# Optimization experiments

Hardware: AMD Instinct MI355X
Metric: run time of the kernel (lower is better)

Reference implementation:

```python
import jax, jax.numpy as jnp
import numpy as np

B, D, T = 256, 128, 512
H = 512
E = 256
WSCALE = 0.05


def setup_inputs() -> dict:
    key = jax.random.key(0)
    ks = jax.random.split(key, 8)
    return {
        "z": jax.random.normal(ks[0], (B, D, T), dtype=jnp.float32),
        "e": jax.random.normal(ks[1], (B, E), dtype=jnp.float32),
        "W_ih": jax.random.normal(ks[2], (3 * H, D), dtype=jnp.float32) * WSCALE,
        "W_hh": jax.random.normal(ks[3], (3 * H, H), dtype=jnp.float32) * WSCALE,
        "b_ih": jax.random.normal(ks[4], (3 * H,), dtype=jnp.float32) * WSCALE,
        "b_hh": jax.random.normal(ks[5], (3 * H,), dtype=jnp.float32) * WSCALE,
        "fc_W": jax.random.normal(ks[6], (D, H), dtype=jnp.float32) * WSCALE,
        "fc_b": jax.random.normal(ks[7], (D,), dtype=jnp.float32) * WSCALE,
    }


def _gru_cell(x, h, W_ih, W_hh, b_ih, b_hh):
    # torch.nn.GRUCell math
    gi = x @ W_ih.T + b_ih  # [B, 3H]
    gh = h @ W_hh.T + b_hh  # [B, 3H]
    i_r, i_z, i_n = jnp.split(gi, 3, axis=-1)
    h_r, h_z, h_n = jnp.split(gh, 3, axis=-1)
    r = jax.nn.sigmoid(i_r + h_r)
    zg = jax.nn.sigmoid(i_z + h_z)
    n = jnp.tanh(i_n + r * h_n)
    return (1.0 - zg) * n + zg * h


def reference(z, e, W_ih, W_hh, b_ih, b_hh, fc_W, fc_b):
    Bd, Dd, Td = z.shape
    Hd = W_hh.shape[1]
    z0 = z[:, :, 0]  # [B, D]
    h0 = jnp.zeros((Bd, Hd), dtype=z.dtype)

    def step(carry, _):
        h_fast, z_prev = carry
        h_fast = _gru_cell(z_prev, h_fast, W_ih, W_hh, b_ih, b_hh)
        delta = h_fast @ fc_W.T + fc_b
        z_t = z_prev + delta
        return (h_fast, z_t), z_t

    _, zs = jax.lax.scan(step, (h0, z0), None, length=Td - 1)  # [T-1, B, D]
    z_hat = jnp.concatenate([z0[None], zs], axis=0)  # [T, B, D]
    return jnp.transpose(z_hat, (1, 2, 0))  # [B, D, T]
```

## Files before the change

### kernel.cpp

```cpp
#include <hip/hip_runtime.h>
#include <hip/hip_fp16.h>

typedef _Float16 f16x8 __attribute__((ext_vector_type(8)));
typedef float f32x4 __attribute__((ext_vector_type(4)));
typedef unsigned long long u64;

#define NT 512
#define B_ 256
#define D_ 128
#define T_ 512
#define H_ 512

#define NG 8
#define CB 32
#define BS 32
#define HS 16
#define DS 4
#define GHSZ (NG * BS * H_)

#define SC  2048.0f
#define S1  (1.0f/2048.0f)
#define S2  (1.0f/4194304.0f)

#define MFMA16(A,B,C) __builtin_amdgcn_mfma_f32_16x16x32_f16((A),(B),(C),0,0,0)
#define ALD(p)   __hip_atomic_load((p),  __ATOMIC_RELAXED, __HIP_MEMORY_SCOPE_AGENT)

__global__ __launch_bounds__(256)
void msd_setup_M(const float* __restrict__ W_ih, const float* __restrict__ fc_W,
                 _Float16* __restrict__ Mhi,
                 _Float16* __restrict__ Mlo)
{
    const int r0 = (blockIdx.x >> 1) * 4;
    const int k  = ((blockIdx.x & 1) << 8) + threadIdx.x;
    for (int rr = 0; rr < 4; ++rr) {
        const int R = r0 + rr;
        const float* wrow = W_ih + (size_t)R * D_;
        float s = 0.0f;
        for (int d = 0; d < D_; ++d) s = fmaf(wrow[d], fc_W[(size_t)d * H_ + k], s);
        _Float16 hi = (_Float16)s;
        _Float16 lo = (_Float16)((s - (float)hi) * SC);
        const int t = R >> 9, jj = R & 511;
        const int c = jj >> 4, l16 = jj & 15;
        const int kt = k >> 5, quad = (k >> 3) & 3, j = k & 7;
        const size_t off = ((size_t)(((c * 3 + t) * 16 + kt) * 16 + l16) * 4 + quad) * 8 + j;
        Mhi[off] = hi;
        Mlo[off] = lo;
    }
}

template<bool L> __device__ __forceinline__ u64 hld(const u64* p) {
    if constexpr (L) return *p;
    else return __hip_atomic_load(p, __ATOMIC_RELAXED, __HIP_MEMORY_SCOPE_AGENT);
}
template<bool L> __device__ __forceinline__ void hst(unsigned short* p, unsigned short v) {
    if constexpr (L) *p = v;
    else __hip_atomic_store(p, v, __ATOMIC_RELAXED, __HIP_MEMORY_SCOPE_AGENT);
}

template<bool L>
__device__ __forceinline__
void run_loop(float* __restrict__ out,
              unsigned short* __restrict__ h1_g, unsigned short* __restrict__ h2_g,
              const _Float16* __restrict__ Mhi_w, const _Float16* __restrict__ Mlo_w,
              unsigned* cg, const unsigned* flgW, volatile unsigned* flgPub,
              const _Float16* Whh_s, const _Float16* WhhL_s, const _Float16* fcW_s,
              float* scr0,
              const int g, const int B0, const int j0, const int d0,
              const int tid, const int lane, const int l16, const int quad,
              const int bh, const int kq, const int bm0,
              const int fcrow, const int* mtb,
              float zfrag, const float* gi0,
              const float* bhh_l, const float* c_l, const float fcb_l)
{
    float gi_st[3] = {gi0[0], gi0[1], gi0[2]};
    float h_own = 0.0f;
    const int ktb = kq * 4;
    const int r_own = bm0 + quad * 4 + kq;
    const size_t a64 = ((size_t)(bm0 + l16) * H_ + quad * 8) >> 2;

    f16x8 Mh[4][3], Ml[4][3];
    #pragma unroll
    for (int ktl = 0; ktl < 4; ++ktl)
        #pragma unroll
        for (int t = 0; t < 3; ++t) {
            Mh[ktl][t] = *(const f16x8*)(Mhi_w + mtb[t] + (ktb + ktl) * 512);
            Ml[ktl][t] = *(const f16x8*)(Mlo_w + mtb[t] + (ktb + ktl) * 512);
        }

    for (int i = 1; i <= T_; ++i) {
        const unsigned tgt = (unsigned)(i - 1);
        if constexpr (L) {
            const volatile unsigned* fp =
                (const volatile unsigned*)(flgW + (lane & 31));
            for (;;) {
                unsigned f = *fp;
                if (__ballot((int)(f >= tgt)) == ~0ull) break;
                asm volatile("buffer_inv" ::: "memory");
            }
            asm volatile("buffer_inv" ::: "memory");
        }

        const size_t rb = (size_t)((i - 1) & 1) * GHSZ + (size_t)g * (BS * H_);
        const size_t wb = (size_t)(i & 1) * GHSZ + (size_t)g * (BS * H_);
        const u64* rh1 = (const u64*)(h1_g + rb);
        const u64* rh2 = (const u64*)(h2_g + rb);

        u64 Ar[4][4];
        #pragma unroll
        for (int ktl = 0; ktl < 4; ++ktl) {
            const int ktg = ktb + ktl;
            Ar[ktl][0] = hld<L>(rh1 + a64 + ktg * 8);
            Ar[ktl][1] = hld<L>(rh1 + a64 + ktg * 8 + 1);
            Ar[ktl][2] = hld<L>(rh2 + a64 + ktg * 8);
            Ar[ktl][3] = hld<L>(rh2 + a64 + ktg * 8 + 1);
        }

        f32x4 acc_gh[3], acc2_gh[3], accM1[3], acc2_gi[3], acc_fc;
        {
            f32x4 z4 = {0.f, 0.f, 0.f, 0.f};
            #pragma unroll
            for (int t = 0; t < 3; ++t) { acc_gh[t] = z4; acc2_gh[t] = z4; accM1[t] = z4; acc2_gi[t] = z4; }
            acc_fc = z4;
        }

        #pragma unroll
        for (int ktl = 0; ktl < 4; ++ktl) {
            const int ktg = ktb + ktl;
            union { u64 q[2]; f16x8 v; } U1, U2;
            U1.q[0] = Ar[ktl][0]; U1.q[1] = Ar[ktl][1];
            U2.q[0] = Ar[ktl][2]; U2.q[1] = Ar[ktl][3];
            f16x8 Ah = U1.v;
            f16x8 Al = U2.v;
            const int chunk = ((ktg * 4 + quad) ^ (l16 & 7)) * 8;
            #pragma unroll
            for (int t = 0; t < 3; ++t) {
                const int row = (t * 16 + l16) * 512 + chunk;
                f16x8 Bwh = *(const f16x8*)(Whh_s + row);
                f16x8 Bwl = *(const f16x8*)(WhhL_s + row);
                acc_gh[t]  = MFMA16(Ah, Bwh, acc_gh[t]);
                acc2_gh[t] = MFMA16(Al, Bwh, acc2_gh[t]);
                acc2_gh[t] = MFMA16(Ah, Bwl, acc2_gh[t]);
                accM1[t]   = MFMA16(Ah, Mh[ktl][t], accM1[t]);
                acc2_gi[t] = MFMA16(Al, Mh[ktl][t], acc2_gi[t]);
                acc2_gi[t] = MFMA16(Ah, Ml[ktl][t], acc2_gi[t]);
            }
            f16x8 Bf = *(const f16x8*)(fcW_s + ((ktg * 4 + quad) ^ fcrow) * 8 + fcrow * 512);
            acc_fc = MFMA16(Ah, Bf, acc_fc);
        }

        float Pgh[3][4], Pgi[3][4], Pfc[4];
        #pragma unroll
        for (int t = 0; t < 3; ++t)
            #pragma unroll
            for (int e = 0; e < 4; ++e) {
                Pgh[t][e] = acc_gh[t][e] * S1 + acc2_gh[t][e] * S2;
                Pgi[t][e] = accM1[t][e] * S1 + acc2_gi[t][e] * S2;
            }
        #pragma unroll
        for (int e = 0; e < 4; ++e) Pfc[e] = acc_fc[e] * S1;

        #pragma unroll
        for (int e = 0; e < 4; ++e) {
            if (e == kq) continue;
            const int si = (kq < e) ? kq : kq - 1;
            float* sp = scr0 + ((((bh * 4 + e) * 3 + si) * 64 + lane) * 9);
            sp[0] = Pgh[0][e]; sp[1] = Pgh[1][e]; sp[2] = Pgh[2][e];
            sp[3] = Pgi[0][e]; sp[4] = Pgi[1][e]; sp[5] = Pgi[2][e];
            sp[6] = Pfc[e];
        }
        __syncthreads();
        float tgh0 = Pgh[0][kq], tgh1 = Pgh[1][kq], tgh2 = Pgh[2][kq];
        float tgi0 = Pgi[0][kq], tgi1 = Pgi[1][kq], tgi2 = Pgi[2][kq];
        float tfc  = Pfc[kq];
        #pragma unroll
        for (int s = 0; s < 3; ++s) {
            const float* sp = scr0 + ((((bh * 4 + kq) * 3 + s) * 64 + lane) * 9);
            tgh0 += sp[0]; tgh1 += sp[1]; tgh2 += sp[2];
            tgi0 += sp[3]; tgi1 += sp[4]; tgi2 += sp[5];
            tfc  += sp[6];
        }

        if (i >= 2) {
            gi_st[0] += tgi0 + c_l[0];
            gi_st[1] += tgi1 + c_l[1];
            gi_st[2] += tgi2 + c_l[2];
            if (l16 < DS) zfrag += tfc + fcb_l;
        }
        if (i <= T_ - 1) {
            float ghr = tgh0 + bhh_l[0];
            float ghz = tgh1 + bhh_l[1];
            float ghn = tgh2 + bhh_l[2];
            float r  = 1.0f / (1.0f + __expf(-(gi_st[0] + ghr)));
            float zg = 1.0f / (1.0f + __expf(-(gi_st[1] + ghz)));
            float xn = gi_st[2] + r * ghn;
            float hn = (1.0f - zg) * tanhf(xn) + zg * h_own;
            h_own = hn;
            const size_t o = (size_t)r_own * H_ + j0 + l16;
            float hs = hn * SC;
            _Float16 a1 = (_Float16)hs;
            _Float16 a2 = (_Float16)((hs - (float)a1) * SC);
            union { _Float16 f; unsigned short u; } c1, c2;
            c1.f = a1; c2.f = a2;
            hst<L>(h1_g + wb + o, c1.u);
            hst<L>(h2_g + wb + o, c2.u);
        }
        __syncthreads();
        if constexpr (L) {
            if (tid == 0) *flgPub = (unsigned)i;
        } else {
            if (tid == 0) {
                __hip_atomic_fetch_add(cg, 1u, __ATOMIC_RELAXED, __HIP_MEMORY_SCOPE_AGENT);
                const unsigned target = (unsigned)(CB * i);
                while (ALD(cg) < target) __builtin_amdgcn_s_sleep(1);
            }
            __syncthreads();
        }
        if (i >= 2 && l16 < DS)
            out[(size_t)(B0 + r_own) * (D_ * T_) + (size_t)(d0 + l16) * T_ + (i - 1)] = zfrag;
    }
}

__global__ __launch_bounds__(NT, 2)
void msd_gru_kernel(const float* __restrict__ zin,
                    const float* __restrict__ W_ih,
                    const float* __restrict__ W_hh,
                    const float* __restrict__ b_ih,
                    const float* __restrict__ b_hh,
                    const float* __restrict__ fc_W,
                    const float* __restrict__ fc_b,
                    float* __restrict__ out,
                    unsigned short* __restrict__ h1_g,
                    unsigned short* __restrict__ h2_g,
                    const _Float16* __restrict__ Mhi_w,
                    const _Float16* __restrict__ Mlo_w,
                    unsigned* __restrict__ cnt)
{
    const int g   = blockIdx.x & 7;
    const int c   = blockIdx.x >> 3;
    const int B0  = g * BS;
    const int j0  = c * HS;
    const int d0  = c * DS;

    const int tid  = threadIdx.x;
    const int wave = tid >> 6;
    const int lane = tid & 63;
    const int l16  = lane & 15;
    const int quad = lane >> 4;
    const int bh   = wave >> 2;
    const int kq   = wave & 3;
    const int bm0  = bh * 16;
    const int r_own = bm0 + quad * 4 + kq;

    __shared__ __attribute__((aligned(16))) _Float16 Whh_s [48 * 512];
    __shared__ __attribute__((aligned(16))) _Float16 WhhL_s[48 * 512];
    __shared__ __attribute__((aligned(16))) _Float16 fcW_s [4 * 512];
    __shared__ __attribute__((aligned(16))) float    scr   [2 * 4 * 3 * 64 * 9];
    __shared__ int mode_s;

    unsigned* xmask = cnt + 640;
    unsigned* ready = cnt + 768;
    if (tid == 0) {
        unsigned xcc;
        asm volatile("s_getreg_b32 %0, hwreg(HW_REG_XCC_ID)" : "=s"(xcc));
        __hip_atomic_fetch_or(xmask + g, 1u << (xcc & 31u), __ATOMIC_RELAXED, __HIP_MEMORY_SCOPE_AGENT);
        __hip_atomic_fetch_add(ready, 1u, __ATOMIC_RELAXED, __HIP_MEMORY_SCOPE_AGENT);
        while (ALD(ready) < (unsigned)(NG * CB)) __builtin_amdgcn_s_sleep(4);
        unsigned m = ALD(xmask + g);
        mode_s = (m & (m - 1u)) ? 1 : 0;
    }

    float* z0s = (float*)Whh_s;
    for (int idx = tid; idx < BS * D_; idx += NT) {
        int b = idx >> 7, d = idx & (D_ - 1);
        z0s[idx] = zin[(size_t)(B0 + b) * (D_ * T_) + (size_t)d * T_];
    }
    __syncthreads();

    float zfrag = (l16 < DS) ? z0s[r_own * D_ + d0 + l16] : 0.0f;
    if (l16 < DS)
        out[(size_t)(B0 + r_own) * (D_ * T_) + (size_t)(d0 + l16) * T_] = zfrag;
    float gi0[3], bhh_l[3], c_l[3];
    for (int t = 0; t < 3; ++t) {
        const int gr = t * H_ + j0 + l16;
        const float* wrow = W_ih + (size_t)gr * D_;
        bhh_l[t] = b_hh[gr];
        float s = b_ih[gr], cc = 0.0f;
        for (int d = 0; d < D_; ++d) {
            float wv = wrow[d];
            cc = fmaf(wv, fc_b[d], cc);
            s  = fmaf(wv, z0s[r_own * D_ + d], s);
        }
        c_l[t] = cc;
        gi0[t] = s;
    }
    const float fcb_l = (l16 < DS) ? fc_b[d0 + l16] : 0.0f;
    __syncthreads();

    for (int idx = tid; idx < 48 * H_; idx += NT) {
        int r = idx >> 9, k = idx & (H_ - 1);
        int gr = (r >> 4) * H_ + j0 + (r & 15);
        int pos = r * 512 + ((((k >> 3) ^ (r & 7)) << 3) | (k & 7));
        float w = W_hh[(size_t)gr * H_ + k];
        _Float16 hi = (_Float16)w;
        Whh_s [pos] = hi;
        WhhL_s[pos] = (_Float16)((w - (float)hi) * SC);
    }
    for (int idx = tid; idx < 4 * H_; idx += NT) {
        int r = idx >> 9, k = idx & (H_ - 1);
        int pos = r * 512 + ((((k >> 3) ^ r) << 3) | (k & 7));
        fcW_s[pos] = (_Float16)fc_W[(size_t)(d0 + r) * H_ + k];
    }
    __syncthreads();

    const int gmode = mode_s;
    const unsigned* flgW = cnt + g * 32;
    volatile unsigned* flgPub = (volatile unsigned*)(cnt + g * 32 + c);
    unsigned* cg = cnt + 256 + g * 32;
    const int fcrow = (l16 < DS) ? l16 : 0;
    int mtb[3];
    #pragma unroll
    for (int t = 0; t < 3; ++t) mtb[t] = ((c * 3 + t) * 16) * 512 + (l16 * 4 + quad) * 8;

    if (gmode == 0)
        run_loop<true >(out, h1_g, h2_g, Mhi_w, Mlo_w, cg, flgW, flgPub,
                        Whh_s, WhhL_s, fcW_s, scr,
                        g, B0, j0, d0, tid, lane, l16, quad, bh, kq, bm0,
                        fcrow, mtb, zfrag, gi0, bhh_l, c_l, fcb_l);
    else
        run_loop<false>(out, h1_g, h2_g, Mhi_w, Mlo_w, cg, flgW, flgPub,
                        Whh_s, WhhL_s, fcW_s, scr,
                        g, B0, j0, d0, tid, lane, l16, quad, bh, kq, bm0,
                        fcrow, mtb, zfrag, gi0, bhh_l, c_l, fcb_l);
}

extern "C" void kernel_launch(void* const* d_in, const int* in_sizes, int n_in,
                              void* d_out, int out_size, void* d_ws, size_t ws_size,
                              hipStream_t stream) {
    const float* z    = (const float*)d_in[0];
    const float* W_ih = (const float*)d_in[2];
    const float* W_hh = (const float*)d_in[3];
    const float* b_ih = (const float*)d_in[4];
    const float* b_hh = (const float*)d_in[5];
    const float* fc_W = (const float*)d_in[6];
    const float* fc_b = (const float*)d_in[7];
    float* out = (float*)d_out;

    char* w = (char*)d_ws;
    unsigned*       cnt = (unsigned*)w;
    unsigned short* h1  = (unsigned short*)(w + 4096);
    unsigned short* h2  = (unsigned short*)(w + 4096 + (size_t)4 * GHSZ);
    _Float16*       Mhi = (_Float16*)(w + 4096 + (size_t)8 * GHSZ);
    _Float16*       Mlo = (_Float16*)(w + 4096 + (size_t)8 * GHSZ + (size_t)3 * H_ * H_ * 2);

    hipMemsetAsync(d_ws, 0, 4096 + (size_t)8 * GHSZ, stream);

    hipLaunchKernelGGL(msd_setup_M, dim3(768), dim3(256), 0, stream, W_ih, fc_W, Mhi, Mlo);
    hipLaunchKernelGGL(msd_gru_kernel, dim3(NG * CB), dim3(NT), 0, stream,
                       z, W_ih, W_hh, b_ih, b_hh, fc_W, fc_b, out, h1, h2, Mhi, Mlo, cnt);
}
```

Before: 2.368 ms.

## Replace per-block step barrier with per-wave write flags and scratch-read flags

Replaces the end-of-step block-wide barrier and single per-block publish flag with per-wave flags. Each wave publishes as soon as its own h stores drain, and a separate flag marks when the block has finished reading the shared scratch, so consumers wait only on the exact producer waves they need. The cross-wave reduction scratch is relaid as two float4 slots per lane for vectorized LDS traffic, and an extra barrier now protects scratch reuse. The flag area in the workspace grows, and correctness depends on the finer-grained memory ordering between waves and blocks.

```diff
diff --git a/kernel.cpp b/kernel.cpp
--- a/kernel.cpp
+++ b/kernel.cpp
@@ -62,7 +62,8 @@
 void run_loop(float* __restrict__ out,
               unsigned short* __restrict__ h1_g, unsigned short* __restrict__ h2_g,
               const _Float16* __restrict__ Mhi_w, const _Float16* __restrict__ Mlo_w,
-              unsigned* cg, const unsigned* flgW, volatile unsigned* flgPub,
+              unsigned* cg, const unsigned* pp,
+              volatile unsigned* fw, volatile unsigned* fr,
               const _Float16* Whh_s, const _Float16* WhhL_s, const _Float16* fcW_s,
               float* scr0,
               const int g, const int B0, const int j0, const int d0,
@@ -90,8 +91,7 @@
     for (int i = 1; i <= T_; ++i) {
         const unsigned tgt = (unsigned)(i - 1);
         if constexpr (L) {
-            const volatile unsigned* fp =
-                (const volatile unsigned*)(flgW + (lane & 31));
+            const volatile unsigned* fp = (const volatile unsigned*)pp;
             for (;;) {
                 unsigned f = *fp;
                 if (__ballot((int)(f >= tgt)) == ~0ull) break;
@@ -163,22 +163,27 @@
         for (int e = 0; e < 4; ++e) {
             if (e == kq) continue;
             const int si = (kq < e) ? kq : kq - 1;
-            float* sp = scr0 + ((((bh * 4 + e) * 3 + si) * 64 + lane) * 9);
-            sp[0] = Pgh[0][e]; sp[1] = Pgh[1][e]; sp[2] = Pgh[2][e];
-            sp[3] = Pgi[0][e]; sp[4] = Pgi[1][e]; sp[5] = Pgi[2][e];
-            sp[6] = Pfc[e];
+            const int slot = (bh * 4 + e) * 3 + si;
+            f32x4 v0 = {Pgh[0][e], Pgh[1][e], Pgh[2][e], Pgi[0][e]};
+            f32x4 v1 = {Pgi[1][e], Pgi[2][e], Pfc[e], 0.0f};
+            *(f32x4*)(scr0 + ((slot * 2 + 0) * 64 + lane) * 4) = v0;
+            *(f32x4*)(scr0 + ((slot * 2 + 1) * 64 + lane) * 4) = v1;
         }
         __syncthreads();
-        float tgh0 = Pgh[0][kq], tgh1 = Pgh[1][kq], tgh2 = Pgh[2][kq];
-        float tgi0 = Pgi[0][kq], tgi1 = Pgi[1][kq], tgi2 = Pgi[2][kq];
-        float tfc  = Pfc[kq];
+        if constexpr (L) {
+            if (tid == 0) *fr = (unsigned)i;
+        }
+        f32x4 r0 = {Pgh[0][kq], Pgh[1][kq], Pgh[2][kq], Pgi[0][kq]};
+        f32x4 r1 = {Pgi[1][kq], Pgi[2][kq], Pfc[kq], 0.0f};
         #pragma unroll
         for (int s = 0; s < 3; ++s) {
-            const float* sp = scr0 + ((((bh * 4 + kq) * 3 + s) * 64 + lane) * 9);
-            tgh0 += sp[0]; tgh1 += sp[1]; tgh2 += sp[2];
-            tgi0 += sp[3]; tgi1 += sp[4]; tgi2 += sp[5];
-            tfc  += sp[6];
-        }
+            const int slot = (bh * 4 + kq) * 3 + s;
+            r0 += *(const f32x4*)(scr0 + ((slot * 2 + 0) * 64 + lane) * 4);
+            r1 += *(const f32x4*)(scr0 + ((slot * 2 + 1) * 64 + lane) * 4);
+        }
+        __syncthreads();
+        const float tgh0 = r0[0], tgh1 = r0[1], tgh2 = r0[2];
+        const float tgi0 = r0[3], tgi1 = r1[0], tgi2 = r1[1], tfc = r1[2];
 
         if (i >= 2) {
             gi_st[0] += tgi0 + c_l[0];
@@ -203,17 +208,18 @@
             c1.f = a1; c2.f = a2;
             hst<L>(h1_g + wb + o, c1.u);
             hst<L>(h2_g + wb + o, c2.u);
-        }
-        __syncthreads();
-        if constexpr (L) {
-            if (tid == 0) *flgPub = (unsigned)i;
-        } else {
-            if (tid == 0) {
-                __hip_atomic_fetch_add(cg, 1u, __ATOMIC_RELAXED, __HIP_MEMORY_SCOPE_AGENT);
-                const unsigned target = (unsigned)(CB * i);
-                while (ALD(cg) < target) __builtin_amdgcn_s_sleep(1);
+            if constexpr (L) {
+                asm volatile("s_waitcnt vmcnt(0)" ::: "memory");
+                if (lane == 0) *fw = (unsigned)i;
+            } else {
+                __syncthreads();
+                if (tid == 0) {
+                    __hip_atomic_fetch_add(cg, 1u, __ATOMIC_RELAXED, __HIP_MEMORY_SCOPE_AGENT);
+                    const unsigned target = (unsigned)(CB * i);
+                    while (ALD(cg) < target) __builtin_amdgcn_s_sleep(1);
+                }
+                __syncthreads();
             }
-            __syncthreads();
         }
         if (i >= 2 && l16 < DS)
             out[(size_t)(B0 + r_own) * (D_ * T_) + (size_t)(d0 + l16) * T_ + (i - 1)] = zfrag;
@@ -254,11 +260,11 @@
     __shared__ __attribute__((aligned(16))) _Float16 Whh_s [48 * 512];
     __shared__ __attribute__((aligned(16))) _Float16 WhhL_s[48 * 512];
     __shared__ __attribute__((aligned(16))) _Float16 fcW_s [4 * 512];
-    __shared__ __attribute__((aligned(16))) float    scr   [2 * 4 * 3 * 64 * 9];
+    __shared__ __attribute__((aligned(16))) float    scr   [24 * 2 * 64 * 4];
     __shared__ int mode_s;
 
-    unsigned* xmask = cnt + 640;
-    unsigned* ready = cnt + 768;
+    unsigned* xmask = cnt + 2432;
+    unsigned* ready = cnt + 2560;
     if (tid == 0) {
         unsigned xcc;
         asm volatile("s_getreg_b32 %0, hwreg(HW_REG_XCC_ID)" : "=s"(xcc));
@@ -269,7 +275,7 @@
         mode_s = (m & (m - 1u)) ? 1 : 0;
     }
 
-    float* z0s = (float*)Whh_s;
+    float* z0s = (float*)scr;
     for (int idx = tid; idx < BS * D_; idx += NT) {
         int b = idx >> 7, d = idx & (D_ - 1);
         z0s[idx] = zin[(size_t)(B0 + b) * (D_ * T_) + (size_t)d * T_];
@@ -313,21 +319,29 @@
     __syncthreads();
 
     const int gmode = mode_s;
-    const unsigned* flgW = cnt + g * 32;
-    volatile unsigned* flgPub = (volatile unsigned*)(cnt + g * 32 + c);
-    unsigned* cg = cnt + 256 + g * 32;
+    const unsigned* pp;
+    {
+        const int l = lane;
+        if (l < 32)
+            pp = cnt + ((((g * CB + (kq * 8 + (l >> 2))) * 2 + bh) << 2) + (l & 3));
+        else
+            pp = cnt + 2048 + g * CB + (l - 32);
+    }
+    volatile unsigned* fw = (volatile unsigned*)(cnt + ((((g * CB + c) * 2 + bh) << 2) + kq));
+    volatile unsigned* fr = (volatile unsigned*)(cnt + 2048 + g * CB + c);
+    unsigned* cg = cnt + 3072 + g * 32;
     const int fcrow = (l16 < DS) ? l16 : 0;
     int mtb[3];
     #pragma unroll
     for (int t = 0; t < 3; ++t) mtb[t] = ((c * 3 + t) * 16) * 512 + (l16 * 4 + quad) * 8;
 
     if (gmode == 0)
-        run_loop<true >(out, h1_g, h2_g, Mhi_w, Mlo_w, cg, flgW, flgPub,
+        run_loop<true >(out, h1_g, h2_g, Mhi_w, Mlo_w, cg, pp, fw, fr,
                         Whh_s, WhhL_s, fcW_s, scr,
                         g, B0, j0, d0, tid, lane, l16, quad, bh, kq, bm0,
                         fcrow, mtb, zfrag, gi0, bhh_l, c_l, fcb_l);
     else
-        run_loop<false>(out, h1_g, h2_g, Mhi_w, Mlo_w, cg, flgW, flgPub,
+        run_loop<false>(out, h1_g, h2_g, Mhi_w, Mlo_w, cg, pp, fw, fr,
                         Whh_s, WhhL_s, fcW_s, scr,
                         g, B0, j0, d0, tid, lane, l16, quad, bh, kq, bm0,
                         fcrow, mtb, zfrag, gi0, bhh_l, c_l, fcb_l);
@@ -347,12 +361,12 @@
 
     char* w = (char*)d_ws;
     unsigned*       cnt = (unsigned*)w;
-    unsigned short* h1  = (unsigned short*)(w + 4096);
-    unsigned short* h2  = (unsigned short*)(w + 4096 + (size_t)4 * GHSZ);
-    _Float16*       Mhi = (_Float16*)(w + 4096 + (size_t)8 * GHSZ);
-    _Float16*       Mlo = (_Float16*)(w + 4096 + (size_t)8 * GHSZ + (size_t)3 * H_ * H_ * 2);
-
-    hipMemsetAsync(d_ws, 0, 4096 + (size_t)8 * GHSZ, stream);
+    unsigned short* h1  = (unsigned short*)(w + 16384);
+    unsigned short* h2  = (unsigned short*)(w + 16384 + (size_t)4 * GHSZ);
+    _Float16*       Mhi = (_Float16*)(w + 16384 + (size_t)8 * GHSZ);
+    _Float16*       Mlo = (_Float16*)(w + 16384 + (size_t)8 * GHSZ + (size_t)3 * H_ * H_ * 2);
+
+    hipMemsetAsync(d_ws, 0, 16384 + (size_t)8 * GHSZ, stream);
 
     hipLaunchKernelGGL(msd_setup_M, dim3(768), dim3(256), 0, stream, W_ih, fc_W, Mhi, Mlo);
     hipLaunchKernelGGL(msd_gru_kernel, dim3(NG * CB), dim3(NT), 0, stream,
```

Measured after the change: 4.165 ms. 1.76x slower.
